# Kernel optimization log

Hardware: AMD Instinct MI355X
Metric: run time of the kernel (lower is better)

Reference implementation:

```python
import jax, jax.numpy as jnp
import numpy as np

B, N, NFG, NFR = 512, 64, 1024, 256
OH, OW = 87, 157
POS_THRESHOLD = 0.2


def setup_inputs() -> dict:
    key = jax.random.key(0)
    ks = jax.random.split(key, 7)
    feats = jax.random.normal(ks[0], (B, N, NFG), dtype=jnp.float32)
    # boxes (x1,y1,x2,y2) in image coordinates
    boxes = jax.random.uniform(ks[1], (B, N, 4), dtype=jnp.float32)
    scale = jnp.array([OW, OH, OW, OH], dtype=jnp.float32)
    boxes = boxes * scale
    s_in = 1.0 / np.sqrt(NFG)
    W_theta = jax.random.normal(ks[2], (NFG, NFR), dtype=jnp.float32) * s_in
    b_theta = jnp.zeros((NFR,), dtype=jnp.float32)
    W_phi = jax.random.normal(ks[3], (NFG, NFR), dtype=jnp.float32) * s_in
    b_phi = jnp.zeros((NFR,), dtype=jnp.float32)
    W_gcn = jax.random.normal(ks[4], (NFG, NFG), dtype=jnp.float32) * s_in
    return {
        "graph_boxes_features": feats,
        "boxes_in_flat": boxes,
        "W_theta": W_theta,
        "b_theta": b_theta,
        "W_phi": W_phi,
        "b_phi": b_phi,
        "W_gcn": W_gcn,
    }


def reference(graph_boxes_features, boxes_in_flat, W_theta, b_theta, W_phi, b_phi, W_gcn):
    nfr = W_theta.shape[-1]
    # box centers [B,N,2]
    cx = (boxes_in_flat[..., 0] + boxes_in_flat[..., 2]) * 0.5
    cy = (boxes_in_flat[..., 1] + boxes_in_flat[..., 3]) * 0.5
    pos = jnp.stack([cx, cy], axis=-1)  # [B,N,2]
    # pairwise euclidean distances [B,N,N]
    diff = pos[:, :, None, :] - pos[:, None, :, :]
    dist = jnp.sqrt(jnp.sum(diff * diff, axis=-1))
    position_mask = dist > (POS_THRESHOLD * OW)

    theta = jnp.einsum('bnf,fr->bnr', graph_boxes_features, W_theta) + b_theta
    phi = jnp.einsum('bnf,fr->bnr', graph_boxes_features, W_phi) + b_phi
    sim = jnp.einsum('bnr,bmr->bnm', theta, phi) / jnp.sqrt(jnp.asarray(nfr, theta.dtype))
    logits = jnp.where(position_mask, -jnp.inf, sim)
    relation_graph = jax.nn.softmax(logits, axis=2)  # [B,N,N]

    agg = jnp.einsum('bnm,bmf->bnf', relation_graph, graph_boxes_features)
    out = jax.nn.relu(jnp.einsum('bnf,fg->bng', agg, W_gcn))
    return out, relation_graph
```

## Files before the change

kernel.cpp:

```cpp
#include <hip/hip_runtime.h>
#include <hip/hip_bf16.h>
#include <math.h>

#define BB   512
#define NN   64
#define NFG  1024
#define NFR  256
#define MM   (BB * NN)
#define RG_OFF 33554432L

typedef __attribute__((ext_vector_type(8))) short bf16x8;
typedef __attribute__((ext_vector_type(4))) float f32x4;
typedef __attribute__((ext_vector_type(8))) unsigned short u16x8;

__device__ inline unsigned short f2bf(float f) {
    union { float f; unsigned u; } v; v.f = f;
    unsigned u = v.u;
    return (unsigned short)((u + 0x7FFFu + ((u >> 16) & 1u)) >> 16);
}

__device__ inline void gld_lds16(const unsigned short* g, unsigned short* l) {
    __builtin_amdgcn_global_load_lds((const __attribute__((address_space(1))) void*)g,
                                     (__attribute__((address_space(3))) void*)l, 16, 0, 0);
}

__device__ inline void wave_fence() {
    asm volatile("" ::: "memory");
    __builtin_amdgcn_wave_barrier();
    __builtin_amdgcn_sched_barrier(0);
}


__device__ void tcast_body(const float* __restrict__ in, unsigned short* __restrict__ out,
                           int K, int N, int bx, int by, float tile[32][33]) {
    const int t  = threadIdx.x;
    const int tx = t & 31, ty = t >> 5;
    const int k0 = by * 32, n0 = bx * 32;
#pragma unroll
    for (int r = 0; r < 4; ++r)
        tile[ty + r * 8][tx] = in[(long)(k0 + ty + r * 8) * N + n0 + tx];
    __syncthreads();
#pragma unroll
    for (int r = 0; r < 4; ++r)
        out[(long)(n0 + ty + r * 8) * K + k0 + tx] = f2bf(tile[tx][ty + r * 8]);
}

__global__ __launch_bounds__(256)
void prep(const float* __restrict__ feats, unsigned short* __restrict__ featsb,
          const float* __restrict__ W_theta, const float* __restrict__ W_phi,
          const float* __restrict__ W_gcn,
          unsigned short* __restrict__ Wtp, unsigned short* __restrict__ Wgt,
          const float* __restrict__ bt, const float* __restrict__ bp,
          float* __restrict__ bias512) {
    __shared__ float tile[32][33];
    const int bid = blockIdx.x;
    const int t   = threadIdx.x;
    if (bid < 16384) {
        long i = ((long)bid * 256 + t) * 8;
        if (i + 8 <= 33554432L) {
            f32x4 a = *(const f32x4*)(feats + i);
            f32x4 b = *(const f32x4*)(feats + i + 4);
            u16x8 o;
#pragma unroll
            for (int c = 0; c < 4; ++c) { o[c] = f2bf(a[c]); o[4 + c] = f2bf(b[c]); }
            *(u16x8*)(featsb + i) = o;
        }
    } else if (bid < 16640) {
        int r = bid - 16384;
        tcast_body(W_theta, Wtp, 1024, 256, r & 7, r >> 3, tile);
    } else if (bid < 16896) {
        int r = bid - 16640;
        tcast_body(W_phi, Wtp + 256 * 1024, 1024, 256, r & 7, r >> 3, tile);
    } else if (bid < 17920) {
        int r = bid - 16896;
        tcast_body(W_gcn, Wgt, 1024, 1024, r & 31, r >> 5, tile);
    } else {
        bias512[t]       = bt[t];
        bias512[t + 256] = bp[t];
    }
}


template<int RELU, int STORE_BF16, int SWIZ, int LOG_FAST>
__global__ __launch_bounds__(256, 4)
void gemm_bt(const unsigned short* __restrict__ A, const unsigned short* __restrict__ Bt,
             const float* __restrict__ bias, void* __restrict__ Cout,
             int M, int N, int K) {
    __shared__ __align__(16) unsigned short As[128 * 64];
    __shared__ __align__(16) unsigned short Bs[128 * 64];
    const int t    = threadIdx.x;
    const int lane = t & 63;
    const int w    = t >> 6;
    const int l15  = lane & 15;
    const int q    = lane >> 4;

    long mtile, ntile;
    if (SWIZ == 1) {
        long linear = (long)blockIdx.y * gridDim.x + blockIdx.x;
        int  xcd  = (int)(linear & 7);
        long slot = linear >> 3;
        mtile = slot & ((1 << LOG_FAST) - 1);
        ntile = (long)xcd * (gridDim.y >> 3) + (slot >> LOG_FAST);
    } else if (SWIZ == 2) {
        long linear = (long)blockIdx.y * gridDim.x + blockIdx.x;
        int  xcd  = (int)(linear & 7);
        long slot = linear >> 3;
        ntile = slot & ((1 << LOG_FAST) - 1);
        mtile = (long)xcd * (gridDim.x >> 3) + (slot >> LOG_FAST);
    } else {
        mtile = blockIdx.x; ntile = blockIdx.y;
    }
    const long tileM = mtile * 128;
    const long tileN = ntile * 128;
    const int wm = (w & 1) * 64;
    const int wn = (w >> 1) * 64;

    f32x4 acc[4][4] = {};

    const int rS = t >> 3;
    const int cS = (t & 7) ^ (rS & 7);
    const unsigned short* gA = A  + (tileM + rS) * (long)K + cS * 8;
    const unsigned short* gB = Bt + (tileN + rS) * (long)K + cS * 8;

    for (int kt = 0; kt < K; kt += 64) {
        __syncthreads();
#pragma unroll
        for (int i = 0; i < 4; ++i) {
            gld_lds16(gA + (long)i * 32 * K + kt, As + (i * 256 + w * 64) * 8);
            gld_lds16(gB + (long)i * 32 * K + kt, Bs + (i * 256 + w * 64) * 8);
        }
        __syncthreads();
#pragma unroll
        for (int ks = 0; ks < 2; ++ks) {
            const int slot = (ks * 4 + q) ^ (l15 & 7);
            bf16x8 af[4], bf[4];
#pragma unroll
            for (int mi = 0; mi < 4; ++mi)
                af[mi] = *(const bf16x8*)(As + (wm + mi * 16 + l15) * 64 + slot * 8);
#pragma unroll
            for (int ni = 0; ni < 4; ++ni)
                bf[ni] = *(const bf16x8*)(Bs + (wn + ni * 16 + l15) * 64 + slot * 8);
#pragma unroll
            for (int mi = 0; mi < 4; ++mi)
#pragma unroll
                for (int ni = 0; ni < 4; ++ni)
                    acc[mi][ni] = __builtin_amdgcn_mfma_f32_16x16x32_bf16(af[mi], bf[ni],
                                                                          acc[mi][ni], 0, 0, 0);
        }
    }

#pragma unroll
    for (int mi = 0; mi < 4; ++mi) {
#pragma unroll
        for (int ni = 0; ni < 4; ++ni) {
            long row0 = tileM + wm + mi * 16 + q * 4;
            long col  = tileN + wn + ni * 16 + l15;
            float bv = bias ? bias[col] : 0.f;
#pragma unroll
            for (int r = 0; r < 4; ++r) {
                float v = acc[mi][ni][r] + bv;
                if (RELU) v = fmaxf(v, 0.f);
                long idx = (row0 + r) * N + col;
                if (STORE_BF16) ((unsigned short*)Cout)[idx] = f2bf(v);
                else            ((float*)Cout)[idx] = v;
            }
        }
    }
}


__global__ __launch_bounds__(256, 4)
void fused_softmax_out(const unsigned short* __restrict__ thetaphi,
                       const float* __restrict__ boxes,
                       const unsigned short* __restrict__ HtT,
                       float* __restrict__ rg_out,
                       float* __restrict__ out) {
    __shared__ __align__(16) float sim_s[64][68];
    __shared__ __align__(16) unsigned short Pb[64][72];
    const int t    = threadIdx.x;
    const int b    = blockIdx.x >> 1;
    const int gh   = blockIdx.x & 1;
    const int lane = t & 63;
    const int w    = t >> 6;
    const int l15  = lane & 15;
    const int q    = lane >> 4;

    const unsigned short* HtB = HtT + (long)b * 64;
    bf16x8 hb0[6], hb1[6];
#pragma unroll
    for (int nt = 0; nt < 6; ++nt) {
        const int g0 = gh * 512 + nt * 16;
        const unsigned short* hp = HtB + (long)(g0 + l15) * 32768 + q * 8;
        hb0[nt] = *(const bf16x8*)(hp);
        hb1[nt] = *(const bf16x8*)(hp + 32);
    }
    __builtin_amdgcn_sched_barrier(0);

    float cx, cy;
    {
        float4 bx = *(const float4*)(boxes + ((long)b * 64 + lane) * 4);
        cx = (bx.x + bx.z) * 0.5f;
        cy = (bx.y + bx.w) * 0.5f;
    }

    {
        f32x4 acc[4] = {};
        const unsigned short* thA = thetaphi + ((long)b * 64 + w * 16 + l15) * 512 + q * 8;
        const unsigned short* thB = thetaphi + ((long)b * 64 + l15) * 512 + 256 + q * 8;
#pragma unroll
        for (int kt = 0; kt < 256; kt += 32) {
            bf16x8 a = *(const bf16x8*)(thA + kt);
#pragma unroll
            for (int ni = 0; ni < 4; ++ni) {
                bf16x8 bb = *(const bf16x8*)(thB + (long)ni * 16 * 512 + kt);
                acc[ni] = __builtin_amdgcn_mfma_f32_16x16x32_bf16(a, bb, acc[ni], 0, 0, 0);
            }
        }
#pragma unroll
        for (int ni = 0; ni < 4; ++ni)
#pragma unroll
            for (int r = 0; r < 4; ++r)
                sim_s[w * 16 + q * 4 + r][ni * 16 + l15] = acc[ni][r] * 0.0625f;
    }
    wave_fence();

    {
        const int i  = t >> 2;
        const int j0 = (t & 3) * 16;
        const float cxi = __shfl(cx, i & 63, 64);
        const float cyi = __shfl(cy, i & 63, 64);
        const float thr = (float)(0.2 * 157.0);
        float vals[16];
        float mx = -__builtin_inff();
#pragma unroll
        for (int jj = 0; jj < 16; ++jj) {
            int j = j0 + jj;
            float dx = cxi - __shfl(cx, j, 64);
            float dy = cyi - __shfl(cy, j, 64);
            bool msk = sqrtf(dx * dx + dy * dy) > thr;
            float s = msk ? -__builtin_inff() : sim_s[i][j];
            vals[jj] = s;
            mx = fmaxf(mx, s);
        }
        mx = fmaxf(mx, __shfl_xor(mx, 1, 64));
        mx = fmaxf(mx, __shfl_xor(mx, 2, 64));
        float sum = 0.f;
#pragma unroll
        for (int jj = 0; jj < 16; ++jj) {
            float e = (vals[jj] == -__builtin_inff()) ? 0.f : __expf(vals[jj] - mx);
            vals[jj] = e;
            sum += e;
        }
        sum += __shfl_xor(sum, 1, 64);
        sum += __shfl_xor(sum, 2, 64);
        float inv = 1.f / sum;
        f32x4 pv[4];
#pragma unroll
        for (int jj = 0; jj < 16; ++jj) {
            float p = vals[jj] * inv;
            pv[jj >> 2][jj & 3] = p;
            Pb[i][j0 + jj] = f2bf(p);
        }
        if (gh == 0) {
            float* rgR = rg_out + ((long)b * 64 + i) * 64 + j0;
#pragma unroll
            for (int c = 0; c < 4; ++c) *(f32x4*)(rgR + c * 4) = pv[c];
        }
    }
    wave_fence();

    {
        bf16x8 af0 = *(const bf16x8*)(&Pb[w * 16 + l15][q * 8]);
        bf16x8 af1 = *(const bf16x8*)(&Pb[w * 16 + l15][32 + q * 8]);
        float* outR = out + (long)b * 65536 + (long)(w * 16 + q * 4) * 1024 + gh * 512 + l15;
#pragma unroll
        for (int nt = 0; nt < 32; ++nt) {
            const int s = nt % 6;
            f32x4 acc = {};
            acc = __builtin_amdgcn_mfma_f32_16x16x32_bf16(af0, hb0[s], acc, 0, 0, 0);
            acc = __builtin_amdgcn_mfma_f32_16x16x32_bf16(af1, hb1[s], acc, 0, 0, 0);
            if (nt + 6 < 32) {
                const int g0 = gh * 512 + (nt + 6) * 16;
                const unsigned short* hp = HtB + (long)(g0 + l15) * 32768 + q * 8;
                hb0[s] = *(const bf16x8*)(hp);
                hb1[s] = *(const bf16x8*)(hp + 32);
            }
#pragma unroll
            for (int r = 0; r < 4; ++r)
                outR[(long)r * 1024 + nt * 16] = fmaxf(acc[r], 0.f);
        }
    }
}


extern "C" void kernel_launch(void* const* d_in, const int* in_sizes, int n_in,
                              void* d_out, int out_size, void* d_ws, size_t ws_size,
                              hipStream_t stream) {
    const float* feats   = (const float*)d_in[0];
    const float* boxes   = (const float*)d_in[1];
    const float* W_theta = (const float*)d_in[2];
    const float* b_theta = (const float*)d_in[3];
    const float* W_phi   = (const float*)d_in[4];
    const float* b_phi   = (const float*)d_in[5];
    const float* W_gcn   = (const float*)d_in[6];
    float* out = (float*)d_out;

    char* ws = (char*)d_ws;
    unsigned short* featsb   = (unsigned short*)(ws);
    unsigned short* thetaphi = (unsigned short*)(ws + 67108864);
    unsigned short* HtT      = (unsigned short*)(ws + 100663296);
    unsigned short* Wtp      = (unsigned short*)(ws + 167772160);
    unsigned short* Wgt      = (unsigned short*)(ws + 168820736);
    float*          bias512  = (float*)(ws + 170917888);

    prep<<<17921, 256, 0, stream>>>(feats, featsb, W_theta, W_phi, W_gcn,
                                    Wtp, Wgt, b_theta, b_phi, bias512);

    gemm_bt<0, 1, 2, 2><<<dim3(256, 4), 256, 0, stream>>>(featsb, Wtp, bias512, thetaphi,
                                                          MM, 512, 1024);
    gemm_bt<0, 1, 1, 3><<<dim3(8, 256), 256, 0, stream>>>(Wgt, featsb, nullptr, HtT,
                                                          1024, MM, 1024);
    fused_softmax_out<<<BB * 2, 256, 0, stream>>>(thetaphi, boxes, HtT, out + RG_OFF, out);
}
```

Before: 416.3 us.

## Replace GEMM with 256x256-tile, 8-wave double-buffered pipelined kernel

```diff
diff --git a/kernel.cpp b/kernel.cpp
--- a/kernel.cpp
+++ b/kernel.cpp
@@ -81,88 +81,119 @@
 }
 
 
-template<int RELU, int STORE_BF16, int SWIZ, int LOG_FAST>
-__global__ __launch_bounds__(256, 4)
-void gemm_bt(const unsigned short* __restrict__ A, const unsigned short* __restrict__ Bt,
-             const float* __restrict__ bias, void* __restrict__ Cout,
-             int M, int N, int K) {
-    __shared__ __align__(16) unsigned short As[128 * 64];
-    __shared__ __align__(16) unsigned short Bs[128 * 64];
+template<int FASTN, int LOGF>
+__global__ __launch_bounds__(512, 2)
+void gemm8p(const unsigned short* __restrict__ A, const unsigned short* __restrict__ Bt,
+            const float* __restrict__ bias, unsigned short* __restrict__ Cout,
+            int M, int N, int K) {
+    __shared__ __align__(16) unsigned short As[2 * 256 * 64];
+    __shared__ __align__(16) unsigned short Bs[2 * 256 * 64];
     const int t    = threadIdx.x;
     const int lane = t & 63;
     const int w    = t >> 6;
     const int l15  = lane & 15;
     const int q    = lane >> 4;
+    const int wm64 = (w >> 2) * 64;
+    const int wn64 = (w & 3) * 64;
 
     long mtile, ntile;
-    if (SWIZ == 1) {
-        long linear = (long)blockIdx.y * gridDim.x + blockIdx.x;
-        int  xcd  = (int)(linear & 7);
-        long slot = linear >> 3;
-        mtile = slot & ((1 << LOG_FAST) - 1);
-        ntile = (long)xcd * (gridDim.y >> 3) + (slot >> LOG_FAST);
-    } else if (SWIZ == 2) {
-        long linear = (long)blockIdx.y * gridDim.x + blockIdx.x;
-        int  xcd  = (int)(linear & 7);
-        long slot = linear >> 3;
-        ntile = slot & ((1 << LOG_FAST) - 1);
-        mtile = (long)xcd * (gridDim.x >> 3) + (slot >> LOG_FAST);
-    } else {
-        mtile = blockIdx.x; ntile = blockIdx.y;
-    }
-    const long tileM = mtile * 128;
-    const long tileN = ntile * 128;
-    const int wm = (w & 1) * 64;
-    const int wn = (w >> 1) * 64;
-
-    f32x4 acc[4][4] = {};
-
-    const int rS = t >> 3;
-    const int cS = (t & 7) ^ (rS & 7);
-    const unsigned short* gA = A  + (tileM + rS) * (long)K + cS * 8;
-    const unsigned short* gB = Bt + (tileN + rS) * (long)K + cS * 8;
-
-    for (int kt = 0; kt < K; kt += 64) {
-        __syncthreads();
-#pragma unroll
-        for (int i = 0; i < 4; ++i) {
-            gld_lds16(gA + (long)i * 32 * K + kt, As + (i * 256 + w * 64) * 8);
-            gld_lds16(gB + (long)i * 32 * K + kt, Bs + (i * 256 + w * 64) * 8);
-        }
-        __syncthreads();
-#pragma unroll
-        for (int ks = 0; ks < 2; ++ks) {
-            const int slot = (ks * 4 + q) ^ (l15 & 7);
-            bf16x8 af[4], bf[4];
-#pragma unroll
-            for (int mi = 0; mi < 4; ++mi)
-                af[mi] = *(const bf16x8*)(As + (wm + mi * 16 + l15) * 64 + slot * 8);
-#pragma unroll
-            for (int ni = 0; ni < 4; ++ni)
-                bf[ni] = *(const bf16x8*)(Bs + (wn + ni * 16 + l15) * 64 + slot * 8);
-#pragma unroll
-            for (int mi = 0; mi < 4; ++mi)
-#pragma unroll
-                for (int ni = 0; ni < 4; ++ni)
-                    acc[mi][ni] = __builtin_amdgcn_mfma_f32_16x16x32_bf16(af[mi], bf[ni],
-                                                                          acc[mi][ni], 0, 0, 0);
-        }
-    }
-
-#pragma unroll
-    for (int mi = 0; mi < 4; ++mi) {
+    {
+        long lin  = blockIdx.x;
+        int  xcd  = (int)(lin & 7);
+        long slot = lin >> 3;
+        long fast = slot & ((1 << LOGF) - 1);
+        long rest = slot >> LOGF;
+        if (FASTN) { ntile = fast; mtile = (long)xcd * ((M >> 8) >> 3) + rest; }
+        else       { mtile = fast; ntile = (long)xcd * ((N >> 8) >> 3) + rest; }
+    }
+    const long tileM = mtile * 256;
+    const long tileN = ntile * 256;
+
+    f32x4 acc[8][4] = {};
+    bf16x8 bfr[2][4];
+
+    const int rT = t >> 3;
+    const int cS = (t & 7) ^ (rT & 7);
+    const unsigned short* gA = A  + (tileM + rT) * (long)K + cS * 8;
+    const unsigned short* gB = Bt + (tileN + rT) * (long)K + cS * 8;
+    const int NT = K >> 6;
+
+    auto stageA = [&](int d, int hf, int j) {
+#pragma unroll
+        for (int i = 0; i < 2; ++i)
+            gld_lds16(gA + (long)(hf * 128 + i * 64) * K + (long)j * 64,
+                      As + d * 16384 + hf * 8192 + i * 4096 + w * 512);
+    };
+    auto stageB = [&](int d, int hf, int j) {
+#pragma unroll
+        for (int i = 0; i < 2; ++i)
+            gld_lds16(gB + (long)(hf * 128 + i * 64) * K + (long)j * 64,
+                      Bs + d * 16384 + hf * 8192 + i * 4096 + w * 512);
+    };
+
+#define PHASE(d, MG, KS, LOADB, STMT) do {                                            \
+    const int slot_ = ((KS) * 4 + q) ^ (l15 & 7);                                     \
+    const unsigned short* Ab_ = As + (d) * 16384;                                     \
+    const unsigned short* Bb_ = Bs + (d) * 16384;                                     \
+    bf16x8 af_[4];                                                                    \
+    _Pragma("unroll")                                                                 \
+    for (int ai = 0; ai < 4; ++ai)                                                    \
+        af_[ai] = *(const bf16x8*)(Ab_ + ((MG) * 128 + wm64 + ai * 16 + l15) * 64 + slot_ * 8); \
+    if (LOADB) {                                                                      \
+        _Pragma("unroll")                                                             \
+        for (int ni = 0; ni < 4; ++ni)                                                \
+            bfr[KS][ni] = *(const bf16x8*)(Bb_ + (wn64 + ni * 16 + l15) * 64 + slot_ * 8);      \
+    }                                                                                 \
+    STMT;                                                                             \
+    __builtin_amdgcn_s_barrier();                                                     \
+    asm volatile("s_waitcnt lgkmcnt(0)" ::: "memory");                                \
+    __builtin_amdgcn_sched_barrier(0);                                                \
+    __builtin_amdgcn_s_setprio(1);                                                    \
+    _Pragma("unroll")                                                                 \
+    for (int ai = 0; ai < 4; ++ai) {                                                  \
+        _Pragma("unroll")                                                             \
+        for (int ni = 0; ni < 4; ++ni)                                                \
+            acc[(MG) * 4 + ai][ni] = __builtin_amdgcn_mfma_f32_16x16x32_bf16(         \
+                af_[ai], bfr[KS][ni], acc[(MG) * 4 + ai][ni], 0, 0, 0);               \
+    }                                                                                 \
+    __builtin_amdgcn_s_setprio(0);                                                    \
+} while (0)
+
+    stageA(0, 0, 0);
+    stageB(0, 0, 0);
+    stageB(0, 1, 0);
+    stageA(0, 1, 0);
+
+    for (int j = 0; j < NT; ++j) {
+        const int d  = j & 1;
+        const int st = (j + 1 < NT);
+        asm volatile("s_waitcnt vmcnt(2)" ::: "memory");
+        __builtin_amdgcn_s_barrier();
+        __builtin_amdgcn_sched_barrier(0);
+        PHASE(d, 0, 0, 1, { if (st) stageA(d ^ 1, 0, j + 1); });
+        __builtin_amdgcn_s_barrier();
+        PHASE(d, 0, 1, 1, { if (st) stageB(d ^ 1, 0, j + 1); });
+        if (j == NT - 1) asm volatile("s_waitcnt vmcnt(0)" ::: "memory");
+        else             asm volatile("s_waitcnt vmcnt(4)" ::: "memory");
+        __builtin_amdgcn_s_barrier();
+        __builtin_amdgcn_sched_barrier(0);
+        PHASE(d, 1, 0, 0, { if (st) stageB(d ^ 1, 1, j + 1); });
+        __builtin_amdgcn_s_barrier();
+        PHASE(d, 1, 1, 0, { if (st) stageA(d ^ 1, 1, j + 1); });
+    }
+#undef PHASE
+
+#pragma unroll
+    for (int a = 0; a < 8; ++a) {
+        long row0 = tileM + (a >> 2) * 128 + wm64 + (a & 3) * 16 + q * 4;
 #pragma unroll
         for (int ni = 0; ni < 4; ++ni) {
-            long row0 = tileM + wm + mi * 16 + q * 4;
-            long col  = tileN + wn + ni * 16 + l15;
+            long col = tileN + wn64 + ni * 16 + l15;
             float bv = bias ? bias[col] : 0.f;
 #pragma unroll
             for (int r = 0; r < 4; ++r) {
-                float v = acc[mi][ni][r] + bv;
-                if (RELU) v = fmaxf(v, 0.f);
-                long idx = (row0 + r) * N + col;
-                if (STORE_BF16) ((unsigned short*)Cout)[idx] = f2bf(v);
-                else            ((float*)Cout)[idx] = v;
+                float v = acc[a][ni][r] + bv;
+                Cout[(row0 + r) * N + col] = f2bf(v);
             }
         }
     }
@@ -316,9 +347,9 @@
     prep<<<17921, 256, 0, stream>>>(feats, featsb, W_theta, W_phi, W_gcn,
                                     Wtp, Wgt, b_theta, b_phi, bias512);
 
-    gemm_bt<0, 1, 2, 2><<<dim3(256, 4), 256, 0, stream>>>(featsb, Wtp, bias512, thetaphi,
-                                                          MM, 512, 1024);
-    gemm_bt<0, 1, 1, 3><<<dim3(8, 256), 256, 0, stream>>>(Wgt, featsb, nullptr, HtT,
-                                                          1024, MM, 1024);
+    gemm8p<1, 1><<<256, 512, 0, stream>>>(featsb, Wtp, bias512, thetaphi,
+                                          MM, 512, 1024);
+    gemm8p<0, 2><<<512, 512, 0, stream>>>(Wgt, featsb, nullptr, HtT,
+                                          1024, MM, 1024);
     fused_softmax_out<<<BB * 2, 256, 0, stream>>>(thetaphi, boxes, HtT, out + RG_OFF, out);
 }
```

After: 415.9 us. About the same (-0.1%).

## Reorder GCN computation to aggregate features first, then apply W_gcn GEMM

Applied to the files above, without the earlier changes.

```diff
diff --git a/kernel.cpp b/kernel.cpp
--- a/kernel.cpp
+++ b/kernel.cpp
@@ -12,6 +12,7 @@
 typedef __attribute__((ext_vector_type(8))) short bf16x8;
 typedef __attribute__((ext_vector_type(4))) float f32x4;
 typedef __attribute__((ext_vector_type(8))) unsigned short u16x8;
+typedef __attribute__((ext_vector_type(4))) unsigned short u16x4;
 
 __device__ inline unsigned short f2bf(float f) {
     union { float f; unsigned u; } v; v.f = f;
@@ -47,32 +48,46 @@
 
 __global__ __launch_bounds__(256)
 void prep(const float* __restrict__ feats, unsigned short* __restrict__ featsb,
+          unsigned short* __restrict__ featsbT,
           const float* __restrict__ W_theta, const float* __restrict__ W_phi,
           const float* __restrict__ W_gcn,
           unsigned short* __restrict__ Wtp, unsigned short* __restrict__ Wgt,
           const float* __restrict__ bt, const float* __restrict__ bp,
           float* __restrict__ bias512) {
+    __shared__ unsigned short tileT[64][80];
     __shared__ float tile[32][33];
     const int bid = blockIdx.x;
     const int t   = threadIdx.x;
-    if (bid < 16384) {
-        long i = ((long)bid * 256 + t) * 8;
-        if (i + 8 <= 33554432L) {
-            f32x4 a = *(const f32x4*)(feats + i);
-            f32x4 b = *(const f32x4*)(feats + i + 4);
-            u16x8 o;
-#pragma unroll
-            for (int c = 0; c < 4; ++c) { o[c] = f2bf(a[c]); o[4 + c] = f2bf(b[c]); }
-            *(u16x8*)(featsb + i) = o;
-        }
-    } else if (bid < 16640) {
-        int r = bid - 16384;
+    if (bid < 8192) {
+        const int i0 = (bid >> 4) * 64, g0 = (bid & 15) * 64;
+        const int tx = t & 15;
+        const int ty = t >> 4;
+#pragma unroll
+        for (int p = 0; p < 4; ++p) {
+            const int row = p * 16 + ty;
+            f32x4 v = *(const f32x4*)(feats + (long)(i0 + row) * 1024 + g0 + tx * 4);
+            u16x4 o;
+#pragma unroll
+            for (int c = 0; c < 4; ++c) o[c] = f2bf(v[c]);
+            *(u16x4*)(featsb + (long)(i0 + row) * 1024 + g0 + tx * 4) = o;
+#pragma unroll
+            for (int c = 0; c < 4; ++c) tileT[tx * 4 + c][row] = o[c];
+        }
+        __syncthreads();
+        const int gr = t >> 2, c0 = (t & 3) * 16;
+        u16x8 w0 = *(const u16x8*)(&tileT[gr][c0]);
+        u16x8 w1 = *(const u16x8*)(&tileT[gr][c0 + 8]);
+        unsigned short* dst = featsbT + (long)(g0 + gr) * 32768 + i0 + c0;
+        *(u16x8*)(dst)     = w0;
+        *(u16x8*)(dst + 8) = w1;
+    } else if (bid < 8448) {
+        int r = bid - 8192;
         tcast_body(W_theta, Wtp, 1024, 256, r & 7, r >> 3, tile);
-    } else if (bid < 16896) {
-        int r = bid - 16640;
+    } else if (bid < 8704) {
+        int r = bid - 8448;
         tcast_body(W_phi, Wtp + 256 * 1024, 1024, 256, r & 7, r >> 3, tile);
-    } else if (bid < 17920) {
-        int r = bid - 16896;
+    } else if (bid < 9728) {
+        int r = bid - 8704;
         tcast_body(W_gcn, Wgt, 1024, 1024, r & 31, r >> 5, tile);
     } else {
         bias512[t]       = bt[t];
@@ -170,11 +185,11 @@
 
 
 __global__ __launch_bounds__(256, 4)
-void fused_softmax_out(const unsigned short* __restrict__ thetaphi,
+void fused_softmax_agg(const unsigned short* __restrict__ thetaphi,
                        const float* __restrict__ boxes,
-                       const unsigned short* __restrict__ HtT,
+                       const unsigned short* __restrict__ fT,
                        float* __restrict__ rg_out,
-                       float* __restrict__ out) {
+                       unsigned short* __restrict__ agg) {
     __shared__ __align__(16) float sim_s[64][68];
     __shared__ __align__(16) unsigned short Pb[64][72];
     const int t    = threadIdx.x;
@@ -185,12 +200,12 @@
     const int l15  = lane & 15;
     const int q    = lane >> 4;
 
-    const unsigned short* HtB = HtT + (long)b * 64;
+    const unsigned short* fTB = fT + (long)b * 64;
     bf16x8 hb0[6], hb1[6];
 #pragma unroll
     for (int nt = 0; nt < 6; ++nt) {
         const int g0 = gh * 512 + nt * 16;
-        const unsigned short* hp = HtB + (long)(g0 + l15) * 32768 + q * 8;
+        const unsigned short* hp = fTB + (long)(g0 + l15) * 32768 + q * 8;
         hb0[nt] = *(const bf16x8*)(hp);
         hb1[nt] = *(const bf16x8*)(hp + 32);
     }
@@ -272,7 +287,8 @@
     {
         bf16x8 af0 = *(const bf16x8*)(&Pb[w * 16 + l15][q * 8]);
         bf16x8 af1 = *(const bf16x8*)(&Pb[w * 16 + l15][32 + q * 8]);
-        float* outR = out + (long)b * 65536 + (long)(w * 16 + q * 4) * 1024 + gh * 512 + l15;
+        unsigned short* aggR = agg + (long)b * 65536 + (long)(w * 16 + q * 4) * 1024
+                                   + gh * 512 + l15;
 #pragma unroll
         for (int nt = 0; nt < 32; ++nt) {
             const int s = nt % 6;
@@ -281,13 +297,13 @@
             acc = __builtin_amdgcn_mfma_f32_16x16x32_bf16(af1, hb1[s], acc, 0, 0, 0);
             if (nt + 6 < 32) {
                 const int g0 = gh * 512 + (nt + 6) * 16;
-                const unsigned short* hp = HtB + (long)(g0 + l15) * 32768 + q * 8;
+                const unsigned short* hp = fTB + (long)(g0 + l15) * 32768 + q * 8;
                 hb0[s] = *(const bf16x8*)(hp);
                 hb1[s] = *(const bf16x8*)(hp + 32);
             }
 #pragma unroll
             for (int r = 0; r < 4; ++r)
-                outR[(long)r * 1024 + nt * 16] = fmaxf(acc[r], 0.f);
+                aggR[(long)r * 1024 + nt * 16] = f2bf(acc[r]);
         }
     }
 }
@@ -308,17 +324,19 @@
     char* ws = (char*)d_ws;
     unsigned short* featsb   = (unsigned short*)(ws);
     unsigned short* thetaphi = (unsigned short*)(ws + 67108864);
-    unsigned short* HtT      = (unsigned short*)(ws + 100663296);
-    unsigned short* Wtp      = (unsigned short*)(ws + 167772160);
-    unsigned short* Wgt      = (unsigned short*)(ws + 168820736);
-    float*          bias512  = (float*)(ws + 170917888);
-
-    prep<<<17921, 256, 0, stream>>>(feats, featsb, W_theta, W_phi, W_gcn,
-                                    Wtp, Wgt, b_theta, b_phi, bias512);
+    unsigned short* featsbT  = (unsigned short*)(ws + 100663296);
+    unsigned short* agg      = (unsigned short*)(ws + 167772160);
+    unsigned short* Wtp      = (unsigned short*)(ws + 234881024);
+    unsigned short* Wgt      = (unsigned short*)(ws + 235929600);
+    float*          bias512  = (float*)(ws + 238026752);
+
+    prep<<<9729, 256, 0, stream>>>(feats, featsb, featsbT, W_theta, W_phi, W_gcn,
+                                   Wtp, Wgt, b_theta, b_phi, bias512);
 
     gemm_bt<0, 1, 2, 2><<<dim3(256, 4), 256, 0, stream>>>(featsb, Wtp, bias512, thetaphi,
                                                           MM, 512, 1024);
-    gemm_bt<0, 1, 1, 3><<<dim3(8, 256), 256, 0, stream>>>(Wgt, featsb, nullptr, HtT,
-                                                          1024, MM, 1024);
-    fused_softmax_out<<<BB * 2, 256, 0, stream>>>(thetaphi, boxes, HtT, out + RG_OFF, out);
-}
+    fused_softmax_agg<<<BB * 2, 256, 0, stream>>>(thetaphi, boxes, featsbT,
+                                                  out + RG_OFF, agg);
+    gemm_bt<1, 0, 2, 3><<<dim3(256, 8), 256, 0, stream>>>(agg, Wgt, nullptr, out,
+                                                          MM, 1024, 1024);
+}
```

Measured after the change: 455.6 us. 1.09x slower.
